# Optimization experiments

Hardware: AMD Instinct MI355X
Metric: run time of the kernel (lower is better)

Reference implementation:

```python
import jax, jax.numpy as jnp
import numpy as np

N_NODES = 50000
N_EDGES = 800000
STATE_DIM = 128
H1 = 96
H2 = 64


def setup_inputs() -> dict:
    key = jax.random.key(0)
    ks = jax.random.split(key, 10)
    x = jax.random.normal(ks[0], (N_NODES, STATE_DIM), dtype=jnp.float32)
    edge_index = jax.random.randint(ks[1], (2, N_EDGES), 0, N_NODES, dtype=jnp.int64)
    # GCNConv weight [in, out] and bias
    W1 = jax.random.normal(ks[2], (STATE_DIM, H1), dtype=jnp.float32) / np.sqrt(STATE_DIM)
    b1 = jnp.zeros((H1,), dtype=jnp.float32)
    lw1 = jax.random.normal(ks[3], (H1, H1), dtype=jnp.float32) / np.sqrt(H1)
    lb1 = jax.random.normal(ks[4], (H1,), dtype=jnp.float32) * 0.01
    lw2 = jax.random.normal(ks[5], (H1, H2), dtype=jnp.float32) / np.sqrt(H1)
    lb2 = jax.random.normal(ks[6], (H2,), dtype=jnp.float32) * 0.01
    lw3 = jax.random.normal(ks[7], (H2, 1), dtype=jnp.float32) / np.sqrt(H2)
    lb3 = jax.random.normal(ks[8], (1,), dtype=jnp.float32) * 0.01
    return {"x": x, "edge_index": edge_index, "W1": W1, "b1": b1,
            "lw1": lw1, "lb1": lb1, "lw2": lw2, "lb2": lb2, "lw3": lw3, "lb3": lb3}


def reference(x, edge_index, W1, b1, lw1, lb1, lw2, lb2, lw3, lb3):
    N = x.shape[0]
    loop = jnp.arange(N, dtype=edge_index.dtype)
    src = jnp.concatenate([edge_index[0], loop])
    dst = jnp.concatenate([edge_index[1], loop])
    deg = jax.ops.segment_sum(jnp.ones_like(dst, dtype=x.dtype), dst, num_segments=N)
    dinv = jnp.where(deg > 0, jax.lax.rsqrt(jnp.maximum(deg, 1.0)), 0.0)
    norm = dinv[src] * dinv[dst]  # [E+N]
    h = x @ W1  # [N, H1] transform before propagation
    agg = jax.ops.segment_sum(h[src] * norm[:, None], dst, num_segments=N) + b1
    out = jax.nn.relu(agg)            # [N, H1]
    g = jnp.sum(out, axis=0)          # sum pooling over nodes -> [H1]
    g = jax.nn.relu(g @ lw1 + lb1)
    g = jax.nn.relu(g @ lw2 + lb2)
    return g @ lw3 + lb3              # [1]
```

## Files before the change

kernel.cpp:

```cpp
#include <hip/hip_runtime.h>
#include <stdint.h>

#define N_NODES 50000
#define N_EDGES 800000
#define D_IN 128
#define H1 96
#define H2 64
#define GEMM_NODES 32
#define GEMM_BLOCKS ((N_NODES + GEMM_NODES - 1) / GEMM_NODES)
#define SCAN_BLK 256
#define N_SBLK ((N_NODES + SCAN_BLK - 1) / SCAN_BLK)
#define SCAT_BLOCKS 2048
#define AGG_BLOCKS 2048

__device__ __forceinline__ int xcd_range(int d) {
    return (int)(((unsigned long long)(unsigned)d * 687195ull) >> 32);
}

__global__ void count_deg_kernel(const int* __restrict__ dst, int* __restrict__ deg) {
    int r = blockIdx.x & 7;
    int gid = (blockIdx.x >> 3) * 256 + threadIdx.x;
    int stride = (SCAT_BLOCKS >> 3) * 256;
    const int4* d4 = (const int4*)dst;
    for (int i = gid; i < N_EDGES / 4; i += stride) {
        int4 d = d4[i];
        if (xcd_range(d.x) == r) atomicAdd(&deg[d.x], 1);
        if (xcd_range(d.y) == r) atomicAdd(&deg[d.y], 1);
        if (xcd_range(d.z) == r) atomicAdd(&deg[d.z], 1);
        if (xcd_range(d.w) == r) atomicAdd(&deg[d.w], 1);
    }
}

__global__ __launch_bounds__(SCAN_BLK) void deg_part_kernel(const int* __restrict__ deg,
                                                            int* __restrict__ block_sums) {
    __shared__ int s[SCAN_BLK];
    int t = threadIdx.x;
    int i = blockIdx.x * SCAN_BLK + t;
    s[t] = (i < N_NODES) ? deg[i] : 0;
    __syncthreads();
    for (int off = SCAN_BLK / 2; off > 0; off >>= 1) {
        if (t < off) s[t] += s[t + off];
        __syncthreads();
    }
    if (t == 0) block_sums[blockIdx.x] = s[0];
}

__global__ __launch_bounds__(SCAN_BLK) void block_scan_kernel(int* __restrict__ block_sums) {
    __shared__ int s[SCAN_BLK];
    int t = threadIdx.x;
    int v = (t < N_SBLK) ? block_sums[t] : 0;
    s[t] = v;
    __syncthreads();
    for (int off = 1; off < SCAN_BLK; off <<= 1) {
        int u = (t >= off) ? s[t - off] : 0;
        __syncthreads();
        s[t] += u;
        __syncthreads();
    }
    if (t < N_SBLK) block_sums[t] = s[t] - v;
}

__global__ __launch_bounds__(SCAN_BLK) void deg_scan_kernel(const int* __restrict__ deg,
                                                            const int* __restrict__ block_off,
                                                            int* __restrict__ row_start,
                                                            int* __restrict__ cursor,
                                                            float* __restrict__ dinv) {
    __shared__ int s[SCAN_BLK];
    int t = threadIdx.x;
    int i = blockIdx.x * SCAN_BLK + t;
    int v = (i < N_NODES) ? deg[i] : 0;
    s[t] = v;
    __syncthreads();
    for (int off = 1; off < SCAN_BLK; off <<= 1) {
        int u = (t >= off) ? s[t - off] : 0;
        __syncthreads();
        s[t] += u;
        __syncthreads();
    }
    int excl = s[t] - v + block_off[blockIdx.x];
    if (i < N_NODES) {
        row_start[i] = excl;
        cursor[i] = excl;
        dinv[i] = rsqrtf((float)v + 1.0f);
    }
    if (i == 0) row_start[N_NODES] = N_EDGES;
}

__global__ __launch_bounds__(256) void k2_scatter_gemm(const int* __restrict__ src,
                                                       const int* __restrict__ dst,
                                                       int* __restrict__ cursor,
                                                       int* __restrict__ sorted_src,
                                                       const float* __restrict__ x,
                                                       const float* __restrict__ W1,
                                                       const float* __restrict__ dinv,
                                                       float* __restrict__ hs) {
    __shared__ float sx[GEMM_NODES * D_IN];
    int tid = threadIdx.x;

    if (blockIdx.x < SCAT_BLOCKS) {
        int r = blockIdx.x & 7;
        int gid = (blockIdx.x >> 3) * 256 + tid;
        int stride = (SCAT_BLOCKS >> 3) * 256;
        const int4* s4p = (const int4*)src;
        const int4* d4p = (const int4*)dst;
        for (int i = gid; i < N_EDGES / 4; i += stride) {
            int4 sv = s4p[i];
            int4 dv = d4p[i];
            if (xcd_range(dv.x) == r) { int p = atomicAdd(&cursor[dv.x], 1); sorted_src[p] = sv.x; }
            if (xcd_range(dv.y) == r) { int p = atomicAdd(&cursor[dv.y], 1); sorted_src[p] = sv.y; }
            if (xcd_range(dv.z) == r) { int p = atomicAdd(&cursor[dv.z], 1); sorted_src[p] = sv.z; }
            if (xcd_range(dv.w) == r) { int p = atomicAdd(&cursor[dv.w], 1); sorted_src[p] = sv.w; }
        }
    } else {
        int gblk = blockIdx.x - SCAT_BLOCKS;
        int base = gblk * GEMM_NODES;
        const float4* x4 = (const float4*)x;
        for (int i = tid; i < GEMM_NODES * D_IN / 4; i += 256) {
            int n = base + i / (D_IN / 4);
            if (n < N_NODES) ((float4*)sx)[i] = x4[(size_t)base * (D_IN / 4) + i];
        }
        __syncthreads();

        int fg = tid & 31;
        int ng = tid >> 5;

        float acc[4][3];
#pragma unroll
        for (int i = 0; i < 4; ++i)
#pragma unroll
            for (int j = 0; j < 3; ++j) acc[i][j] = 0.0f;

#pragma unroll 4
        for (int k = 0; k < D_IN; ++k) {
            float w0 = W1[k * H1 + fg];
            float w1 = W1[k * H1 + fg + 32];
            float w2 = W1[k * H1 + fg + 64];
#pragma unroll
            for (int i = 0; i < 4; ++i) {
                float xv = sx[(ng * 4 + i) * D_IN + k];
                acc[i][0] = fmaf(xv, w0, acc[i][0]);
                acc[i][1] = fmaf(xv, w1, acc[i][1]);
                acc[i][2] = fmaf(xv, w2, acc[i][2]);
            }
        }

#pragma unroll
        for (int i = 0; i < 4; ++i) {
            int n = base + ng * 4 + i;
            if (n < N_NODES) {
                float dv = dinv[n];
                hs[(size_t)n * H1 + fg]      = acc[i][0] * dv;
                hs[(size_t)n * H1 + fg + 32] = acc[i][1] * dv;
                hs[(size_t)n * H1 + fg + 64] = acc[i][2] * dv;
            }
        }
    }
}

__global__ __launch_bounds__(256) void agg_pool_kernel(const float* __restrict__ hs,
                                                       const int* __restrict__ row_start,
                                                       const int* __restrict__ sorted_src,
                                                       const float* __restrict__ dinv,
                                                       const float* __restrict__ b1,
                                                       float* __restrict__ g) {
    int tid = threadIdx.x;
    int grp = tid >> 7;
    int f = tid & 127;
    bool act = f < H1;
    float bf = act ? b1[f] : 0.0f;
    float gacc = 0.0f;

    for (int n = blockIdx.x * 2 + grp; n < N_NODES; n += gridDim.x * 2) {
        float acc = act ? hs[(size_t)n * H1 + f] : 0.0f;
        int e = row_start[n];
        int eend = row_start[n + 1];
        for (; e + 4 <= eend; e += 4) {
            int s0 = sorted_src[e];
            int s1 = sorted_src[e + 1];
            int s2 = sorted_src[e + 2];
            int s3 = sorted_src[e + 3];
            if (act) {
                float v0 = hs[(size_t)s0 * H1 + f];
                float v1 = hs[(size_t)s1 * H1 + f];
                float v2 = hs[(size_t)s2 * H1 + f];
                float v3 = hs[(size_t)s3 * H1 + f];
                acc += (v0 + v1) + (v2 + v3);
            }
        }
        for (; e < eend; ++e) {
            int s = sorted_src[e];
            if (act) acc += hs[(size_t)s * H1 + f];
        }
        if (act) gacc += fmaxf(fmaf(dinv[n], acc, bf), 0.0f);
    }

    __shared__ float sg[H1];
    if (grp == 0 && act) sg[f] = gacc;
    __syncthreads();
    if (grp == 1 && act) atomicAdd(&sg[f], gacc);
    __syncthreads();
    if (grp == 0 && act) atomicAdd(&g[f], sg[f]);
}

__global__ __launch_bounds__(256) void mlp_kernel(const float* __restrict__ g,
                           const float* __restrict__ lw1, const float* __restrict__ lb1,
                           const float* __restrict__ lw2, const float* __restrict__ lb2,
                           const float* __restrict__ lw3, const float* __restrict__ lb3,
                           float* __restrict__ out) {
    __shared__ float slw1[H1 * H1];
    __shared__ float slw2[H1 * H2];
    __shared__ float slw3[H2];
    __shared__ float sg[H1], v1[H1], v2[H2];
    int t = threadIdx.x;
    for (int i = t; i < H1 * H1 / 4; i += 256)
        ((float4*)slw1)[i] = ((const float4*)lw1)[i];
    for (int i = t; i < H1 * H2 / 4; i += 256)
        ((float4*)slw2)[i] = ((const float4*)lw2)[i];
    if (t < H2) slw3[t] = lw3[t];
    if (t < H1) sg[t] = g[t];
    __syncthreads();
    if (t < H1) {
        float a = lb1[t];
#pragma unroll 8
        for (int k = 0; k < H1; ++k) a = fmaf(sg[k], slw1[k * H1 + t], a);
        v1[t] = fmaxf(a, 0.0f);
    }
    __syncthreads();
    if (t < H2) {
        float a = lb2[t];
#pragma unroll 8
        for (int k = 0; k < H1; ++k) a = fmaf(v1[k], slw2[k * H2 + t], a);
        v2[t] = fmaxf(a, 0.0f);
    }
    __syncthreads();
    if (t == 0) {
        float a = lb3[0];
#pragma unroll 8
        for (int k = 0; k < H2; ++k) a = fmaf(v2[k], slw3[k], a);
        out[0] = a;
    }
}

extern "C" void kernel_launch(void* const* d_in, const int* in_sizes, int n_in,
                              void* d_out, int out_size, void* d_ws, size_t ws_size,
                              hipStream_t stream) {
    const float* x   = (const float*)d_in[0];
    const int*   ei  = (const int*)d_in[1];
    const float* W1  = (const float*)d_in[2];
    const float* b1  = (const float*)d_in[3];
    const float* lw1 = (const float*)d_in[4];
    const float* lb1 = (const float*)d_in[5];
    const float* lw2 = (const float*)d_in[6];
    const float* lb2 = (const float*)d_in[7];
    const float* lw3 = (const float*)d_in[8];
    const float* lb3 = (const float*)d_in[9];
    float* out = (float*)d_out;

    const int* src = ei;
    const int* dst = ei + N_EDGES;

    char* ws = (char*)d_ws;
    size_t off = 0;
    auto alloc = [&](size_t bytes) {
        char* p = ws + off;
        off = (off + bytes + 255) & ~(size_t)255;
        return p;
    };
    int*   deg        = (int*)alloc((size_t)N_NODES * sizeof(int));
    float* g          = (float*)alloc((size_t)H1 * sizeof(float));
    float* dinv       = (float*)alloc((size_t)N_NODES * sizeof(float));
    int*   row_start  = (int*)alloc((size_t)(N_NODES + 1) * sizeof(int));
    int*   cursor     = (int*)alloc((size_t)N_NODES * sizeof(int));
    int*   block_sums = (int*)alloc((size_t)N_SBLK * sizeof(int));
    int*   sorted_src = (int*)alloc((size_t)N_EDGES * sizeof(int));
    float* hs         = (float*)alloc((size_t)N_NODES * H1 * sizeof(float));
    (void)ws_size;

    hipMemsetAsync(deg, 0, (char*)(g + H1) - (char*)deg, stream);

    count_deg_kernel<<<SCAT_BLOCKS, 256, 0, stream>>>(dst, deg);
    deg_part_kernel<<<N_SBLK, SCAN_BLK, 0, stream>>>(deg, block_sums);
    block_scan_kernel<<<1, SCAN_BLK, 0, stream>>>(block_sums);
    deg_scan_kernel<<<N_SBLK, SCAN_BLK, 0, stream>>>(deg, block_sums, row_start, cursor, dinv);

    k2_scatter_gemm<<<SCAT_BLOCKS + GEMM_BLOCKS, 256, 0, stream>>>(src, dst, cursor, sorted_src,
                                                                   x, W1, dinv, hs);

    agg_pool_kernel<<<AGG_BLOCKS, 256, 0, stream>>>(hs, row_start, sorted_src, dinv, b1, g);

    mlp_kernel<<<1, 256, 0, stream>>>(g, lw1, lb1, lw2, lb2, lw3, lb3, out);
}
```

Measured before the change: 226.7 us.

## Move GEMM into degree-count kernel and scale by dinv during scatter

The dense X·W1 GEMM now shares a launch with the degree-count atomics, so the two independent stages overlap. The GEMM no longer needs dinv, which is only known after the scan. The dinv row scaling becomes a separate elementwise pass over h that runs alongside the CSR scatter. In exchange, h is read and written once more (about 19 MB each way), and the count work now competes with GEMM blocks in the same launch.

```diff
diff --git a/kernel.cpp b/kernel.cpp
--- a/kernel.cpp
+++ b/kernel.cpp
@@ -8,26 +8,79 @@
 #define H2 64
 #define GEMM_NODES 32
 #define GEMM_BLOCKS ((N_NODES + GEMM_NODES - 1) / GEMM_NODES)
+#define COUNT_BLOCKS 2048
 #define SCAN_BLK 256
 #define N_SBLK ((N_NODES + SCAN_BLK - 1) / SCAN_BLK)
 #define SCAT_BLOCKS 2048
+#define SCALE_BLOCKS 512
 #define AGG_BLOCKS 2048
 
 __device__ __forceinline__ int xcd_range(int d) {
     return (int)(((unsigned long long)(unsigned)d * 687195ull) >> 32);
 }
 
-__global__ void count_deg_kernel(const int* __restrict__ dst, int* __restrict__ deg) {
-    int r = blockIdx.x & 7;
-    int gid = (blockIdx.x >> 3) * 256 + threadIdx.x;
-    int stride = (SCAT_BLOCKS >> 3) * 256;
-    const int4* d4 = (const int4*)dst;
-    for (int i = gid; i < N_EDGES / 4; i += stride) {
-        int4 d = d4[i];
-        if (xcd_range(d.x) == r) atomicAdd(&deg[d.x], 1);
-        if (xcd_range(d.y) == r) atomicAdd(&deg[d.y], 1);
-        if (xcd_range(d.z) == r) atomicAdd(&deg[d.z], 1);
-        if (xcd_range(d.w) == r) atomicAdd(&deg[d.w], 1);
+__global__ __launch_bounds__(256) void k1_gemm_count(const float* __restrict__ x,
+                                                     const float* __restrict__ W1,
+                                                     float* __restrict__ h,
+                                                     const int* __restrict__ dst,
+                                                     int* __restrict__ deg) {
+    __shared__ float sx[GEMM_NODES * D_IN];
+    int tid = threadIdx.x;
+
+    if (blockIdx.x < GEMM_BLOCKS) {
+        int base = blockIdx.x * GEMM_NODES;
+        const float4* x4 = (const float4*)x;
+        for (int i = tid; i < GEMM_NODES * D_IN / 4; i += 256) {
+            int n = base + i / (D_IN / 4);
+            if (n < N_NODES) ((float4*)sx)[i] = x4[(size_t)base * (D_IN / 4) + i];
+        }
+        __syncthreads();
+
+        int fg = tid & 31;
+        int ng = tid >> 5;
+
+        float acc[4][3];
+#pragma unroll
+        for (int i = 0; i < 4; ++i)
+#pragma unroll
+            for (int j = 0; j < 3; ++j) acc[i][j] = 0.0f;
+
+#pragma unroll 4
+        for (int k = 0; k < D_IN; ++k) {
+            float w0 = W1[k * H1 + fg];
+            float w1 = W1[k * H1 + fg + 32];
+            float w2 = W1[k * H1 + fg + 64];
+#pragma unroll
+            for (int i = 0; i < 4; ++i) {
+                float xv = sx[(ng * 4 + i) * D_IN + k];
+                acc[i][0] = fmaf(xv, w0, acc[i][0]);
+                acc[i][1] = fmaf(xv, w1, acc[i][1]);
+                acc[i][2] = fmaf(xv, w2, acc[i][2]);
+            }
+        }
+
+#pragma unroll
+        for (int i = 0; i < 4; ++i) {
+            int n = base + ng * 4 + i;
+            if (n < N_NODES) {
+                h[(size_t)n * H1 + fg]      = acc[i][0];
+                h[(size_t)n * H1 + fg + 32] = acc[i][1];
+                h[(size_t)n * H1 + fg + 64] = acc[i][2];
+            }
+        }
+    } else {
+        int r = blockIdx.x & 7;
+        int bid = blockIdx.x - GEMM_BLOCKS;
+        int gid = (bid >> 3) * 256 + tid;
+        int stride = (COUNT_BLOCKS >> 3) * 256;
+        const int4* d4 = (const int4*)dst;
+        for (int i = gid; i < N_EDGES / 4; i += stride) {
+            int4 d = d4[i];
+            if (xcd_range(d.x) == r) atomicAdd(&deg[d.x], 1);
+            if (xcd_range(d.y) == r) atomicAdd(&deg[d.y], 1);
+            if (xcd_range(d.z) == r) atomicAdd(&deg[d.z], 1);
+            if (xcd_range(d.w) == r) atomicAdd(&deg[d.w], 1);
+        }
     }
 }
 
@@ -86,17 +139,13 @@
     if (i == 0) row_start[N_NODES] = N_EDGES;
 }
 
-__global__ __launch_bounds__(256) void k2_scatter_gemm(const int* __restrict__ src,
-                                                       const int* __restrict__ dst,
-                                                       int* __restrict__ cursor,
-                                                       int* __restrict__ sorted_src,
-                                                       const float* __restrict__ x,
-                                                       const float* __restrict__ W1,
-                                                       const float* __restrict__ dinv,
-                                                       float* __restrict__ hs) {
-    __shared__ float sx[GEMM_NODES * D_IN];
+__global__ __launch_bounds__(256) void k2_scatter_scale(const int* __restrict__ src,
+                                                        const int* __restrict__ dst,
+                                                        int* __restrict__ cursor,
+                                                        int* __restrict__ sorted_src,
+                                                        float* __restrict__ h,
+                                                        const float* __restrict__ dinv) {
     int tid = threadIdx.x;
-
     if (blockIdx.x < SCAT_BLOCKS) {
         int r = blockIdx.x & 7;
         int gid = (blockIdx.x >> 3) * 256 + tid;
@@ -112,47 +161,17 @@
             if (xcd_range(dv.w) == r) { int p = atomicAdd(&cursor[dv.w], 1); sorted_src[p] = sv.w; }
         }
     } else {
-        int gblk = blockIdx.x - SCAT_BLOCKS;
-        int base = gblk * GEMM_NODES;
-        const float4* x4 = (const float4*)x;
-        for (int i = tid; i < GEMM_NODES * D_IN / 4; i += 256) {
-            int n = base + i / (D_IN / 4);
-            if (n < N_NODES) ((float4*)sx)[i] = x4[(size_t)base * (D_IN / 4) + i];
-        }
-        __syncthreads();
-
-        int fg = tid & 31;
-        int ng = tid >> 5;
-
-        float acc[4][3];
-#pragma unroll
-        for (int i = 0; i < 4; ++i)
-#pragma unroll
-            for (int j = 0; j < 3; ++j) acc[i][j] = 0.0f;
-
-#pragma unroll 4
-        for (int k = 0; k < D_IN; ++k) {
-            float w0 = W1[k * H1 + fg];
-            float w1 = W1[k * H1 + fg + 32];
-            float w2 = W1[k * H1 + fg + 64];
-#pragma unroll
-            for (int i = 0; i < 4; ++i) {
-                float xv = sx[(ng * 4 + i) * D_IN + k];
-                acc[i][0] = fmaf(xv, w0, acc[i][0]);
-                acc[i][1] = fmaf(xv, w1, acc[i][1]);
-                acc[i][2] = fmaf(xv, w2, acc[i][2]);
-            }
-        }
-
-#pragma unroll
-        for (int i = 0; i < 4; ++i) {
-            int n = base + ng * 4 + i;
-            if (n < N_NODES) {
-                float dv = dinv[n];
-                hs[(size_t)n * H1 + fg]      = acc[i][0] * dv;
-                hs[(size_t)n * H1 + fg + 32] = acc[i][1] * dv;
-                hs[(size_t)n * H1 + fg + 64] = acc[i][2] * dv;
-            }
+        int bid = blockIdx.x - SCAT_BLOCKS;
+        int gid = bid * 256 + tid;
+        int stride = SCALE_BLOCKS * 256;
+        float4* h4 = (float4*)h;
+        const int TOT = N_NODES * (H1 / 4);
+        for (int i = gid; i < TOT; i += stride) {
+            int n = i / (H1 / 4);
+            float dv = dinv[n];
+            float4 v = h4[i];
+            v.x *= dv; v.y *= dv; v.z *= dv; v.w *= dv;
+            h4[i] = v;
         }
     }
 }
@@ -273,20 +292,21 @@
     int*   cursor     = (int*)alloc((size_t)N_NODES * sizeof(int));
     int*   block_sums = (int*)alloc((size_t)N_SBLK * sizeof(int));
     int*   sorted_src = (int*)alloc((size_t)N_EDGES * sizeof(int));
-    float* hs         = (float*)alloc((size_t)N_NODES * H1 * sizeof(float));
+    float* h          = (float*)alloc((size_t)N_NODES * H1 * sizeof(float));
     (void)ws_size;
 
     hipMemsetAsync(deg, 0, (char*)(g + H1) - (char*)deg, stream);
 
-    count_deg_kernel<<<SCAT_BLOCKS, 256, 0, stream>>>(dst, deg);
+    k1_gemm_count<<<GEMM_BLOCKS + COUNT_BLOCKS, 256, 0, stream>>>(x, W1, h, dst, deg);
+
     deg_part_kernel<<<N_SBLK, SCAN_BLK, 0, stream>>>(deg, block_sums);
     block_scan_kernel<<<1, SCAN_BLK, 0, stream>>>(block_sums);
     deg_scan_kernel<<<N_SBLK, SCAN_BLK, 0, stream>>>(deg, block_sums, row_start, cursor, dinv);
 
-    k2_scatter_gemm<<<SCAT_BLOCKS + GEMM_BLOCKS, 256, 0, stream>>>(src, dst, cursor, sorted_src,
-                                                                   x, W1, dinv, hs);
-
-    agg_pool_kernel<<<AGG_BLOCKS, 256, 0, stream>>>(hs, row_start, sorted_src, dinv, b1, g);
+    k2_scatter_scale<<<SCAT_BLOCKS + SCALE_BLOCKS, 256, 0, stream>>>(src, dst, cursor, sorted_src,
+                                                                     h, dinv);
+
+    agg_pool_kernel<<<AGG_BLOCKS, 256, 0, stream>>>(h, row_start, sorted_src, dinv, b1, g);
 
     mlp_kernel<<<1, 256, 0, stream>>>(g, lw1, lb1, lw2, lb2, lw3, lb3, out);
 }
```

Result: faster. 207.9 us (-8.3%).
